# Kernel tuning notes

Hardware: AMD Instinct MI355X
Metric: run time of the kernel (lower is better)

The kernel has to match this reference:

```python
import jax, jax.numpy as jnp
import numpy as np

N_NODES, N_EDGES, D, M_BLOCKS = 50000, 800000, 128, 4  # nodes, edges, feat dim, mp_iterations
EPS = 1e-5


def setup_inputs() -> dict:
    key = jax.random.key(0)
    ks = jax.random.split(key, 16)

    def p(k, shape):
        return jax.random.normal(k, shape, dtype=jnp.float32) * 0.05

    return {
        "x": jax.random.normal(ks[0], (N_NODES, D), dtype=jnp.float32),
        "edge_attr": jax.random.normal(ks[1], (N_EDGES, D), dtype=jnp.float32),
        # Edge MLP params per block: Linear(3D->D), Linear(D->D), Linear(D->D), LayerNorm(D)
        "ew1": p(ks[2], (M_BLOCKS, 3 * D, D)), "eb1": jnp.zeros((M_BLOCKS, D), jnp.float32),
        "ew2": p(ks[3], (M_BLOCKS, D, D)),     "eb2": jnp.zeros((M_BLOCKS, D), jnp.float32),
        "ew3": p(ks[4], (M_BLOCKS, D, D)),     "eb3": jnp.zeros((M_BLOCKS, D), jnp.float32),
        "eg": jnp.ones((M_BLOCKS, D), jnp.float32), "ebeta": jnp.zeros((M_BLOCKS, D), jnp.float32),
        # Node MLP params per block: Linear(2D->D), Linear(D->D), Linear(D->D), LayerNorm(D)
        "nw1": p(ks[5], (M_BLOCKS, 2 * D, D)), "nb1": jnp.zeros((M_BLOCKS, D), jnp.float32),
        "nw2": p(ks[6], (M_BLOCKS, D, D)),     "nb2": jnp.zeros((M_BLOCKS, D), jnp.float32),
        "nw3": p(ks[7], (M_BLOCKS, D, D)),     "nb3": jnp.zeros((M_BLOCKS, D), jnp.float32),
        "ng": jnp.ones((M_BLOCKS, D), jnp.float32), "nbeta": jnp.zeros((M_BLOCKS, D), jnp.float32),
        "edge_index": jax.random.randint(ks[8], (2, N_EDGES), 0, N_NODES, dtype=jnp.int32),
    }


def _layernorm(h, g, b):
    mu = jnp.mean(h, axis=-1, keepdims=True)
    var = jnp.mean((h - mu) ** 2, axis=-1, keepdims=True)
    return (h - mu) * jax.lax.rsqrt(var + EPS) * g + b


def _mlp(h, w1, b1, w2, b2, w3, b3, g, beta):
    h = jax.nn.relu(h @ w1 + b1)
    h = jax.nn.relu(h @ w2 + b2)
    h = h @ w3 + b3
    return _layernorm(h, g, beta)


def reference(x, edge_attr, ew1, eb1, ew2, eb2, ew3, eb3, eg, ebeta,
              nw1, nb1, nw2, nb2, nw3, nb3, ng, nbeta, edge_index):
    n_nodes = x.shape[0]
    row, col = edge_index[0], edge_index[1]

    # NOTE: the original torch loop never reassigns x/edge_attr, so every block
    # consumes the original inputs; only the last block's (residual) output is kept.
    def step(carry, p):
        (pew1, peb1, pew2, peb2, pew3, peb3, peg, pebeta,
         pnw1, pnb1, pnw2, pnb2, pnw3, pnb3, png, pnbeta) = p
        # Edge update: gather src/dst node feats, concat with edge feats -> MLP
        e_in = jnp.concatenate([x[row], x[col], edge_attr], axis=-1)  # [E, 3D]
        e = _mlp(e_in, pew1, peb1, pew2, peb2, pew3, peb3, peg, pebeta)  # [E, D]
        # Node update: scatter-sum edges onto destination nodes, concat -> MLP
        agg = jax.ops.segment_sum(e, col, num_segments=n_nodes)  # [N, D]
        n_in = jnp.concatenate([x, agg], axis=-1)  # [N, 2D]
        nx = _mlp(n_in, pnw1, pnb1, pnw2, pnb2, pnw3, pnb3, png, pnbeta)  # [N, D]
        return (nx + x, e + edge_attr), None

    stacked = (ew1, eb1, ew2, eb2, ew3, eb3, eg, ebeta,
               nw1, nb1, nw2, nb2, nw3, nb3, ng, nbeta)
    (out_x, out_e), _ = jax.lax.scan(step, (x, edge_attr), stacked)
    return out_x, out_e
```

## Files before the change

kernel.cpp:

```cpp
#include <hip/hip_runtime.h>
#include <cstdint>
#include <cstddef>

#define D 128
#define NEDGE 800000
#define NNODE 50000

typedef __attribute__((ext_vector_type(8))) short short8;
typedef __attribute__((ext_vector_type(4))) float f32x4;

__device__ __forceinline__ unsigned short f2bf(float f) {
  return (unsigned short)((__float_as_uint(f) + 0x8000u) >> 16);
}
__device__ __forceinline__ unsigned pack2(float lo, float hi) {
  return __builtin_amdgcn_perm(__float_as_uint(hi) + 0x8000u,
                               __float_as_uint(lo) + 0x8000u, 0x07060302u);
}
__device__ __forceinline__ void gl_lds16(const void* g, void* l) {
  __builtin_amdgcn_global_load_lds(
      (const __attribute__((address_space(1))) unsigned*)g,
      (__attribute__((address_space(3))) unsigned*)l, 16, 0, 0);
}

__global__ void prep_weights(const float* __restrict__ ew1, const float* __restrict__ ew2,
                             const float* __restrict__ ew3, const float* __restrict__ nw1,
                             const float* __restrict__ nw2, const float* __restrict__ nw3,
                             unsigned short* __restrict__ img) {
  int t = blockIdx.x * 256 + threadIdx.x;
  int kk = t & 31;
  int n  = (t >> 5) & 127;
  int c  = t >> 12;
  if (c >= 36) return;
  const float* src; int cl; int ioff;
  if      (c < 12) { src = ew1; cl = c;      ioff = 0;      }
  else if (c < 16) { src = ew2; cl = c - 12; ioff = 61440;  }
  else if (c < 20) { src = ew3; cl = c - 16; ioff = 81920;  }
  else if (c < 28) { src = nw1; cl = c - 20; ioff = 102400; }
  else if (c < 32) { src = nw2; cl = c - 28; ioff = 143360; }
  else             { src = nw3; cl = c - 32; ioff = 163840; }
  img[ioff + (cl * 128 + n) * 40 + kk] = f2bf(src[(cl * 32 + kk) * 128 + n]);
}

template <int NCH, bool EDGE>
__global__ __launch_bounds__(256, 2)
void mlp_fused(const float* __restrict__ srcA,
               const float* __restrict__ srcB,
               const int* __restrict__ rowidx, const int* __restrict__ colidx,
               const unsigned short* __restrict__ w1,
               const unsigned short* __restrict__ w2,
               const unsigned short* __restrict__ w3,
               const float* __restrict__ b1, const float* __restrict__ b2,
               const float* __restrict__ b3,
               const float* __restrict__ gam, const float* __restrict__ bet,
               float* __restrict__ outp, float* __restrict__ agg, int M) {
  __shared__ __align__(16) char lds[77824];
  char*  sStage = lds;
  char*  sH     = lds + 40960;
  float* sStats = (float*)(lds + 75776);

  const int tid  = threadIdx.x;
  const int wave = tid >> 6, lane = tid & 63;
  const int wm = wave >> 1, wn = wave & 1;
  const int lr = lane & 15, lq = lane >> 4;
  const int m0 = blockIdx.x * 128;

  const int sr = tid >> 1;
  const int ssub = tid & 1;
  const float* pA0; const float* pA1; const float* pA2 = nullptr;
  bool svalid = true;
  if (EDGE) {
    int e = m0 + sr;
    pA0 = srcA + (size_t)rowidx[e] * D;
    pA1 = srcA + (size_t)colidx[e] * D;
    pA2 = srcB + (size_t)e * D;
  } else {
    int node = m0 + sr;
    svalid = node < M;
    pA0 = srcA + (size_t)node * D;
    pA1 = srcB + (size_t)node * D;
  }

  float4 av[4];
  auto loadA = [&](int kc) {
    const float* base;
    if (EDGE) base = (kc < 4) ? pA0 + kc * 32
                   : (kc < 8) ? pA1 + (kc - 4) * 32
                              : pA2 + (kc - 8) * 32;
    else      base = (kc < 4) ? pA0 + kc * 32 : pA1 + (kc - 4) * 32;
    if (!EDGE && !svalid) {
#pragma unroll
      for (int i = 0; i < 4; i++) av[i] = make_float4(0.f, 0.f, 0.f, 0.f);
    } else {
#pragma unroll
      for (int i = 0; i < 4; i++) av[i] = *(const float4*)(base + ssub * 16 + i * 4);
    }
  };
  auto storeA = [&](int bb) {
    char* dst = sStage + bb * 10240 + (sr * 40 + ssub * 16) * 2;
#pragma unroll
    for (int i = 0; i < 4; i++) {
      uint2 pk;
      pk.x = pack2(av[i].x, av[i].y);
      pk.y = pack2(av[i].z, av[i].w);
      *(uint2*)(dst + i * 8) = pk;
    }
  };
  auto stageB = [&](int bb, int kc) {
    const char* g = (const char*)w1 + kc * 10240;
    char* l = sStage + 20480 + bb * 10240;
    for (int s = wave; s < 10; s += 4) gl_lds16(g + s * 1024 + lane * 16, l + s * 1024);
  };
  auto stageFull = [&](const unsigned short* w) {
    for (int s = wave; s < 40; s += 4)
      gl_lds16((const char*)w + s * 1024 + lane * 16, sStage + s * 1024);
  };

  const f32x4 fz = {0.f, 0.f, 0.f, 0.f};
  f32x4 acc[4][4];
#pragma unroll
  for (int mt = 0; mt < 4; mt++)
#pragma unroll
    for (int nt = 0; nt < 4; nt++) acc[mt][nt] = fz;

  loadA(0); storeA(0); stageB(0, 0);
  __syncthreads();
  for (int kc = 0; kc < NCH; kc++) {
    int cur = kc & 1;
    if (kc + 1 < NCH) { stageB(cur ^ 1, kc + 1); loadA(kc + 1); }
    {
      const char* pa = sStage + cur * 10240;
      const char* pb = sStage + 20480 + cur * 10240;
      short8 a[4], b[4];
#pragma unroll
      for (int t2 = 0; t2 < 4; t2++) {
        a[t2] = *(const short8*)(pa + (wm * 64 + t2 * 16 + lr) * 80 + lq * 16);
        b[t2] = *(const short8*)(pb + (wn * 64 + t2 * 16 + lr) * 80 + lq * 16);
      }
#pragma unroll
      for (int mt = 0; mt < 4; mt++)
#pragma unroll
        for (int nt = 0; nt < 4; nt++)
          acc[mt][nt] = __builtin_amdgcn_mfma_f32_16x16x32_bf16(a[mt], b[nt], acc[mt][nt], 0, 0, 0);
    }
    if (kc + 1 < NCH) storeA(cur ^ 1);
    __syncthreads();
  }

  {
    float bb[4];
#pragma unroll
    for (int nt = 0; nt < 4; nt++) bb[nt] = b1[wn * 64 + nt * 16 + lr];
#pragma unroll
    for (int mt = 0; mt < 4; mt++) {
      int row = wm * 64 + mt * 16 + lq * 4;
#pragma unroll
      for (int nt = 0; nt < 4; nt++) {
        int col = wn * 64 + nt * 16 + lr;
#pragma unroll
        for (int r = 0; r < 4; r++) {
          float v = fmaxf(acc[mt][nt][r] + bb[nt], 0.f);
          *(unsigned short*)(sH + ((row + r) * 136 + col) * 2) = f2bf(v);
        }
      }
    }
  }
  stageFull(w2);
  __syncthreads();

#pragma unroll
  for (int mt = 0; mt < 4; mt++)
#pragma unroll
    for (int nt = 0; nt < 4; nt++) acc[mt][nt] = fz;
#pragma unroll
  for (int kc = 0; kc < 4; kc++) {
    short8 a[4], b[4];
#pragma unroll
    for (int t2 = 0; t2 < 4; t2++) {
      a[t2] = *(const short8*)(sH + (wm * 64 + t2 * 16 + lr) * 272 + kc * 64 + lq * 16);
      b[t2] = *(const short8*)(sStage + kc * 10240 + (wn * 64 + t2 * 16 + lr) * 80 + lq * 16);
    }
#pragma unroll
    for (int mt = 0; mt < 4; mt++)
#pragma unroll
      for (int nt = 0; nt < 4; nt++)
        acc[mt][nt] = __builtin_amdgcn_mfma_f32_16x16x32_bf16(a[mt], b[nt], acc[mt][nt], 0, 0, 0);
  }
  __syncthreads();
  {
    float bb[4];
#pragma unroll
    for (int nt = 0; nt < 4; nt++) bb[nt] = b2[wn * 64 + nt * 16 + lr];
#pragma unroll
    for (int mt = 0; mt < 4; mt++) {
      int row = wm * 64 + mt * 16 + lq * 4;
#pragma unroll
      for (int nt = 0; nt < 4; nt++) {
        int col = wn * 64 + nt * 16 + lr;
#pragma unroll
        for (int r = 0; r < 4; r++) {
          float v = fmaxf(acc[mt][nt][r] + bb[nt], 0.f);
          *(unsigned short*)(sH + ((row + r) * 136 + col) * 2) = f2bf(v);
        }
      }
    }
  }
  stageFull(w3);
  __syncthreads();

#pragma unroll
  for (int mt = 0; mt < 4; mt++)
#pragma unroll
    for (int nt = 0; nt < 4; nt++) acc[mt][nt] = fz;
#pragma unroll
  for (int kc = 0; kc < 4; kc++) {
    short8 a[4], b[4];
#pragma unroll
    for (int t2 = 0; t2 < 4; t2++) {
      a[t2] = *(const short8*)(sH + (wm * 64 + t2 * 16 + lr) * 272 + kc * 64 + lq * 16);
      b[t2] = *(const short8*)(sStage + kc * 10240 + (wn * 64 + t2 * 16 + lr) * 80 + lq * 16);
    }
#pragma unroll
    for (int mt = 0; mt < 4; mt++)
#pragma unroll
      for (int nt = 0; nt < 4; nt++)
        acc[mt][nt] = __builtin_amdgcn_mfma_f32_16x16x32_bf16(a[mt], b[nt], acc[mt][nt], 0, 0, 0);
  }

  float b3v[4], gv[4], bev[4]; int colv[4];
#pragma unroll
  for (int nt = 0; nt < 4; nt++) {
    int col = wn * 64 + nt * 16 + lr;
    colv[nt] = col;
    b3v[nt] = b3[col]; gv[nt] = gam[col]; bev[nt] = bet[col];
  }
#pragma unroll
  for (int mt = 0; mt < 4; mt++) {
#pragma unroll
    for (int r = 0; r < 4; r++) {
      float s = 0.f, ss = 0.f;
#pragma unroll
      for (int nt = 0; nt < 4; nt++) {
        float v = acc[mt][nt][r] + b3v[nt];
        acc[mt][nt][r] = v;
        s += v; ss += v * v;
      }
#pragma unroll
      for (int o = 1; o < 16; o <<= 1) { s += __shfl_xor(s, o); ss += __shfl_xor(ss, o); }
      if (lr == 0) {
        int row = wm * 64 + mt * 16 + lq * 4 + r;
        sStats[(row * 2 + wn) * 2 + 0] = s;
        sStats[(row * 2 + wn) * 2 + 1] = ss;
      }
    }
  }
  __syncthreads();
#pragma unroll
  for (int mt = 0; mt < 4; mt++) {
#pragma unroll
    for (int r = 0; r < 4; r++) {
      int row = wm * 64 + mt * 16 + lq * 4 + r;
      int gm = m0 + row;
      float s  = sStats[(row * 2 + 0) * 2 + 0] + sStats[(row * 2 + 1) * 2 + 0];
      float ss = sStats[(row * 2 + 0) * 2 + 1] + sStats[(row * 2 + 1) * 2 + 1];
      float mean = s * (1.f / 128.f);
      float var  = ss * (1.f / 128.f) - mean * mean;
      float rstd = rsqrtf(var + 1e-5f);
      if (EDGE) {
        int cv = colidx[gm];
        float* aggrow = agg + (size_t)cv * D;
        const float* res = srcB + (size_t)gm * D;
        float* orow = outp + (size_t)gm * D;
#pragma unroll
        for (int nt = 0; nt < 4; nt++) {
          int col = colv[nt];
          float e = (acc[mt][nt][r] - mean) * rstd * gv[nt] + bev[nt];
          atomicAdd(aggrow + col, e);
          orow[col] = e + res[col];
        }
      } else if (gm < M) {
        const float* res = srcA + (size_t)gm * D;
        float* orow = outp + (size_t)gm * D;
#pragma unroll
        for (int nt = 0; nt < 4; nt++) {
          int col = colv[nt];
          float e = (acc[mt][nt][r] - mean) * rstd * gv[nt] + bev[nt];
          orow[col] = e + res[col];
        }
      }
    }
  }
}

extern "C" void kernel_launch(void* const* d_in, const int* in_sizes, int n_in,
                              void* d_out, int out_size, void* d_ws, size_t ws_size,
                              hipStream_t stream) {
  const float* x   = (const float*)d_in[0];
  const float* ea  = (const float*)d_in[1];
  const float* ew1 = (const float*)d_in[2]  + 3 * 384 * 128;
  const float* eb1 = (const float*)d_in[3]  + 3 * 128;
  const float* ew2 = (const float*)d_in[4]  + 3 * 128 * 128;
  const float* eb2 = (const float*)d_in[5]  + 3 * 128;
  const float* ew3 = (const float*)d_in[6]  + 3 * 128 * 128;
  const float* eb3 = (const float*)d_in[7]  + 3 * 128;
  const float* eg  = (const float*)d_in[8]  + 3 * 128;
  const float* ebt = (const float*)d_in[9]  + 3 * 128;
  const float* nw1 = (const float*)d_in[10] + 3 * 256 * 128;
  const float* nb1 = (const float*)d_in[11] + 3 * 128;
  const float* nw2 = (const float*)d_in[12] + 3 * 128 * 128;
  const float* nb2 = (const float*)d_in[13] + 3 * 128;
  const float* nw3 = (const float*)d_in[14] + 3 * 128 * 128;
  const float* nb3 = (const float*)d_in[15] + 3 * 128;
  const float* ng  = (const float*)d_in[16] + 3 * 128;
  const float* nbt = (const float*)d_in[17] + 3 * 128;
  const int* rowi  = (const int*)d_in[18];
  const int* coli  = rowi + NEDGE;

  float* agg = (float*)d_ws;
  unsigned short* img = (unsigned short*)((char*)d_ws + 25600000);

  float* outx = (float*)d_out;
  float* oute = outx + (size_t)NNODE * D;

  hipMemsetAsync(agg, 0, (size_t)NNODE * D * sizeof(float), stream);
  prep_weights<<<576, 256, 0, stream>>>(ew1, ew2, ew3, nw1, nw2, nw3, img);
  mlp_fused<12, true><<<NEDGE / 128, 256, 0, stream>>>(
      x, ea, rowi, coli, img + 0, img + 61440, img + 81920,
      eb1, eb2, eb3, eg, ebt, oute, agg, NEDGE);
  mlp_fused<8, false><<<(NNODE + 127) / 128, 256, 0, stream>>>(
      x, agg, nullptr, nullptr, img + 102400, img + 143360, img + 163840,
      nb1, nb2, nb3, ng, nbt, outx, nullptr, NNODE);
}
```

Before: 1.277 ms.

## Read layer-2/3 weights directly from global memory and halve LDS footprint

```diff
diff --git a/kernel.cpp b/kernel.cpp
--- a/kernel.cpp
+++ b/kernel.cpp
@@ -31,18 +31,20 @@
   int n  = (t >> 5) & 127;
   int c  = t >> 12;
   if (c >= 36) return;
-  const float* src; int cl; int ioff;
-  if      (c < 12) { src = ew1; cl = c;      ioff = 0;      }
-  else if (c < 16) { src = ew2; cl = c - 12; ioff = 61440;  }
-  else if (c < 20) { src = ew3; cl = c - 16; ioff = 81920;  }
-  else if (c < 28) { src = nw1; cl = c - 20; ioff = 102400; }
-  else if (c < 32) { src = nw2; cl = c - 28; ioff = 143360; }
-  else             { src = nw3; cl = c - 32; ioff = 163840; }
-  img[ioff + (cl * 128 + n) * 40 + kk] = f2bf(src[(cl * 32 + kk) * 128 + n]);
+  const float* src; int cl; int ioff; bool plain;
+  if      (c < 12) { src = ew1; cl = c;      ioff = 0;      plain = false; }
+  else if (c < 16) { src = ew2; cl = c - 12; ioff = 61440;  plain = true;  }
+  else if (c < 20) { src = ew3; cl = c - 16; ioff = 77824;  plain = true;  }
+  else if (c < 28) { src = nw1; cl = c - 20; ioff = 94208;  plain = false; }
+  else if (c < 32) { src = nw2; cl = c - 28; ioff = 135168; plain = true;  }
+  else             { src = nw3; cl = c - 32; ioff = 151552; plain = true;  }
+  unsigned short v = f2bf(src[(cl * 32 + kk) * 128 + n]);
+  if (plain) img[ioff + n * 128 + cl * 32 + kk] = v;
+  else       img[ioff + (cl * 128 + n) * 40 + kk] = v;
 }
 
 template <int NCH, bool EDGE>
-__global__ __launch_bounds__(256, 2)
+__global__ __launch_bounds__(256, 4)
 void mlp_fused(const float* __restrict__ srcA,
                const float* __restrict__ srcB,
                const int* __restrict__ rowidx, const int* __restrict__ colidx,
@@ -53,10 +55,10 @@
                const float* __restrict__ b3,
                const float* __restrict__ gam, const float* __restrict__ bet,
                float* __restrict__ outp, float* __restrict__ agg, int M) {
-  __shared__ __align__(16) char lds[77824];
+  __shared__ __align__(16) char lds[40960];
   char*  sStage = lds;
-  char*  sH     = lds + 40960;
-  float* sStats = (float*)(lds + 75776);
+  char*  sH     = lds;
+  float* sStats = (float*)(lds + 34816);
 
   const int tid  = threadIdx.x;
   const int wave = tid >> 6, lane = tid & 63;
@@ -110,10 +112,6 @@
     char* l = sStage + 20480 + bb * 10240;
     for (int s = wave; s < 10; s += 4) gl_lds16(g + s * 1024 + lane * 16, l + s * 1024);
   };
-  auto stageFull = [&](const unsigned short* w) {
-    for (int s = wave; s < 40; s += 4)
-      gl_lds16((const char*)w + s * 1024 + lane * 16, sStage + s * 1024);
-  };
 
   const f32x4 fz = {0.f, 0.f, 0.f, 0.f};
   f32x4 acc[4][4];
@@ -146,6 +144,11 @@
     __syncthreads();
   }
 
+  int boff[4];
+#pragma unroll
+  for (int t2 = 0; t2 < 4; t2++)
+    boff[t2] = ((wn * 64 + t2 * 16 + lr) * 128 + lq * 8) * 2;
+
   {
     float bb[4];
 #pragma unroll
@@ -164,7 +167,6 @@
       }
     }
   }
-  stageFull(w2);
   __syncthreads();
 
 #pragma unroll
@@ -177,7 +179,7 @@
 #pragma unroll
     for (int t2 = 0; t2 < 4; t2++) {
       a[t2] = *(const short8*)(sH + (wm * 64 + t2 * 16 + lr) * 272 + kc * 64 + lq * 16);
-      b[t2] = *(const short8*)(sStage + kc * 10240 + (wn * 64 + t2 * 16 + lr) * 80 + lq * 16);
+      b[t2] = *(const short8*)((const char*)w2 + boff[t2] + kc * 64);
     }
 #pragma unroll
     for (int mt = 0; mt < 4; mt++)
@@ -204,7 +206,6 @@
       }
     }
   }
-  stageFull(w3);
   __syncthreads();
 
 #pragma unroll
@@ -217,7 +218,7 @@
 #pragma unroll
     for (int t2 = 0; t2 < 4; t2++) {
       a[t2] = *(const short8*)(sH + (wm * 64 + t2 * 16 + lr) * 272 + kc * 64 + lq * 16);
-      b[t2] = *(const short8*)(sStage + kc * 10240 + (wn * 64 + t2 * 16 + lr) * 80 + lq * 16);
+      b[t2] = *(const short8*)((const char*)w3 + boff[t2] + kc * 64);
     }
 #pragma unroll
     for (int mt = 0; mt < 4; mt++)
@@ -324,9 +325,9 @@
   hipMemsetAsync(agg, 0, (size_t)NNODE * D * sizeof(float), stream);
   prep_weights<<<576, 256, 0, stream>>>(ew1, ew2, ew3, nw1, nw2, nw3, img);
   mlp_fused<12, true><<<NEDGE / 128, 256, 0, stream>>>(
-      x, ea, rowi, coli, img + 0, img + 61440, img + 81920,
+      x, ea, rowi, coli, img + 0, img + 61440, img + 77824,
       eb1, eb2, eb3, eg, ebt, oute, agg, NEDGE);
   mlp_fused<8, false><<<(NNODE + 127) / 128, 256, 0, stream>>>(
-      x, agg, nullptr, nullptr, img + 102400, img + 143360, img + 163840,
+      x, agg, nullptr, nullptr, img + 94208, img + 135168, img + 151552,
       nb1, nb2, nb3, ng, nbt, outx, nullptr, NNODE);
 }
```

Measured after the change: 1.332 ms. 4.3% more time.
